# Kernel tuning notes

Hardware: AMD Instinct MI355X
Metric: run time of the kernel (lower is better)

Reference implementation:

```python
import jax, jax.numpy as jnp
import numpy as np
from jax import lax

B, CIN, H, W = 32, 256, 28, 28
COUT, KS, KEXP = 256, 3, 4
HIDDEN = int(CIN * 0.25)  # ratio hard-coded to 0.25 in the module


def setup_inputs() -> dict:
    key = jax.random.key(0)
    k1, k2, k3, k4 = jax.random.split(key, 4)
    x = jax.random.normal(k1, (B, CIN, H, W), dtype=jnp.float32)
    # SE (InvertedEx) params: fc1 (1x1 conv, no bias), fc2 (1x1 conv, bias)
    fc1_w = jax.random.normal(k2, (HIDDEN, CIN), dtype=jnp.float32) * np.float32(np.sqrt(2.0 / CIN))
    fc2_w = jax.random.normal(k3, (KEXP * COUT, HIDDEN), dtype=jnp.float32) * np.float32(np.sqrt(2.0 / HIDDEN))
    fc2_b = jnp.zeros((KEXP * COUT,), dtype=jnp.float32)
    # K expert conv kernels, he_std = sqrt(2) * (CIN*KS^2)^-0.5
    he_std = np.float32(np.sqrt(2.0) * (CIN * KS * KS) ** -0.5)
    weight = jax.random.normal(k4, (KEXP, COUT, CIN, KS, KS), dtype=jnp.float32) * he_std
    return {"x": x, "fc1_w": fc1_w, "fc2_w": fc2_w, "fc2_b": fc2_b, "weight": weight}


def reference(x, fc1_w, fc2_w, fc2_b, weight):
    # --- SE routing ---
    pooled = jnp.mean(x, axis=(2, 3))                        # [B, CIN]
    h = jax.nn.relu(pooled @ fc1_w.T)                        # [B, HIDDEN]
    y = (h @ fc2_w.T + fc2_b).reshape(B, KEXP, COUT)         # [B, K, COUT]
    prob = jax.nn.softmax(y / jnp.sqrt(jnp.float32(HIDDEN)), axis=1)  # softmax over K
    # --- aggregate per-sample kernels ---
    agg_w = jnp.einsum('bko,koihw->boihw', prob, weight)     # [B, COUT, CIN, KS, KS]
    # --- per-sample conv (batched implicit GEMM via vmap) ---
    def conv1(xi, wi):
        return lax.conv_general_dilated(
            xi[None], wi, window_strides=(1, 1), padding=((1, 1), (1, 1)),
            dimension_numbers=('NCHW', 'OIHW', 'NCHW'))[0]
    out = jax.vmap(conv1)(x, agg_w)                          # [B, COUT, H, W]
    return out
```

## Files before the change

kernel.cpp:

```cpp
#include <hip/hip_runtime.h>
#include <math.h>

#define B_    32
#define CIN_  256
#define HW_   784
#define H_    28
#define W_    28
#define COUT_ 256
#define KEXP_ 4
#define HID_  64

typedef short short8 __attribute__((ext_vector_type(8)));
typedef unsigned short ushort4v __attribute__((ext_vector_type(4)));
typedef unsigned short ushort8v __attribute__((ext_vector_type(8)));
typedef float floatx16 __attribute__((ext_vector_type(16)));

__device__ __forceinline__ unsigned short f2bf(float f) {
    union { float f; unsigned int u; } v; v.f = f;
    unsigned int r = (v.u + 0x7FFFu + ((v.u >> 16) & 1u)) >> 16;
    return (unsigned short)r;
}

__global__ __launch_bounds__(256) void xpose_pool_kernel(const float* __restrict__ x,
                                                         unsigned short* __restrict__ x_t,
                                                         float* __restrict__ partial) {
    __shared__ float tile[32][33];
    int bid = blockIdx.x;
    int b   = bid / 200;
    int rem = bid - b * 200;
    int icg = rem / 25;
    int pxt = rem % 25;
    int ic0 = icg * 32;
    int px0 = pxt * 32;
    int t = threadIdx.x;
    int c = t & 31, rr = t >> 5;
    #pragma unroll
    for (int r = 0; r < 4; ++r) {
        int icr = rr + r * 8;
        int px = px0 + c;
        float v = (px < HW_) ? x[((size_t)(b * CIN_ + ic0 + icr)) * HW_ + px] : 0.f;
        tile[icr][c] = v;
    }
    __syncthreads();
    #pragma unroll
    for (int r = 0; r < 4; ++r) {
        int pxr = rr + r * 8;
        int px = px0 + pxr;
        if (px < HW_)
            x_t[((size_t)b * HW_ + px) * CIN_ + ic0 + c] = f2bf(tile[c][pxr]);
    }
    if (t < 32) {
        float s = 0.f;
        #pragma unroll
        for (int cc = 0; cc < 32; ++cc) s += tile[t][cc];
        partial[((size_t)b * 25 + pxt) * CIN_ + ic0 + t] = s * (1.0f / HW_);
    }
}

__global__ __launch_bounds__(256) void pool_kernel(const float* __restrict__ x,
                                                   float* __restrict__ pooled) {
    int w = blockIdx.x * 4 + (threadIdx.x >> 6);
    int lane = threadIdx.x & 63;
    const float* p = x + (size_t)w * HW_;
    float s = 0.f;
    for (int i = lane; i < HW_; i += 64) s += p[i];
    for (int off = 32; off; off >>= 1) s += __shfl_down(s, off);
    if (lane == 0) pooled[w] = s * (1.0f / HW_);
}

__global__ __launch_bounds__(256) void se3_kernel(const float* __restrict__ partial,
                                                  const float* __restrict__ fc1_w,
                                                  const float* __restrict__ fc2_w,
                                                  const float* __restrict__ fc2_b,
                                                  float* __restrict__ prob) {
    __shared__ float pl[CIN_];
    __shared__ float h[HID_];
    __shared__ float wb[16640];
    int b = blockIdx.x, t = threadIdx.x;
    {
        float s = 0.f;
        for (int pt = 0; pt < 25; ++pt)
            s += partial[((size_t)b * 25 + pt) * CIN_ + t];
        pl[t] = s;
    }
    #pragma unroll
    for (int i = 0; i < 16; ++i) {
        int l = t + i * 256;
        float4 v = *(const float4*)(fc1_w + (size_t)l * 4);
        int r = l >> 6, cc = (l & 63) * 4;
        float* dst = &wb[r * 257 + cc];
        dst[0] = v.x; dst[1] = v.y; dst[2] = v.z; dst[3] = v.w;
    }
    __syncthreads();
    if (t < HID_) {
        float s = 0.f;
        const float* wr = &wb[t * 257];
        for (int c = 0; c < CIN_; ++c) s += pl[c] * wr[c];
        h[t] = fmaxf(s, 0.f);
    }
    float yk[KEXP_];
    for (int k = 0; k < KEXP_; ++k) {
        __syncthreads();
        #pragma unroll
        for (int i = 0; i < 16; ++i) {
            int l = t + i * 256;
            float4 v = *(const float4*)(fc2_w + (size_t)k * COUT_ * HID_ + (size_t)l * 4);
            int o = l >> 4, jj = (l & 15) * 4;
            float* dst = &wb[o * 65 + jj];
            dst[0] = v.x; dst[1] = v.y; dst[2] = v.z; dst[3] = v.w;
        }
        __syncthreads();
        float s = fc2_b[k * COUT_ + t];
        const float* wr = &wb[t * 65];
        #pragma unroll
        for (int j = 0; j < HID_; ++j) s += h[j] * wr[j];
        yk[k] = s * 0.125f;
    }
    float m = yk[0];
    for (int k = 1; k < KEXP_; ++k) m = fmaxf(m, yk[k]);
    float e[KEXP_], sum = 0.f;
    for (int k = 0; k < KEXP_; ++k) { e[k] = expf(yk[k] - m); sum += e[k]; }
    float inv = 1.0f / sum;
    for (int k = 0; k < KEXP_; ++k)
        prob[b * (KEXP_ * COUT_) + k * COUT_ + t] = e[k] * inv;
}

__global__ __launch_bounds__(256) void se2_kernel(const float* __restrict__ pooled,
                                                  const float* __restrict__ fc1_w,
                                                  const float* __restrict__ fc2_w,
                                                  const float* __restrict__ fc2_b,
                                                  float* __restrict__ prob) {
    __shared__ float pl[CIN_];
    __shared__ float h[HID_];
    __shared__ float wb[16640];
    int b = blockIdx.x, t = threadIdx.x;
    pl[t] = pooled[b * CIN_ + t];
    #pragma unroll
    for (int i = 0; i < 16; ++i) {
        int l = t + i * 256;
        float4 v = *(const float4*)(fc1_w + (size_t)l * 4);
        int r = l >> 6, cc = (l & 63) * 4;
        float* dst = &wb[r * 257 + cc];
        dst[0] = v.x; dst[1] = v.y; dst[2] = v.z; dst[3] = v.w;
    }
    __syncthreads();
    if (t < HID_) {
        float s = 0.f;
        const float* wr = &wb[t * 257];
        for (int c = 0; c < CIN_; ++c) s += pl[c] * wr[c];
        h[t] = fmaxf(s, 0.f);
    }
    float yk[KEXP_];
    for (int k = 0; k < KEXP_; ++k) {
        __syncthreads();
        #pragma unroll
        for (int i = 0; i < 16; ++i) {
            int l = t + i * 256;
            float4 v = *(const float4*)(fc2_w + (size_t)k * COUT_ * HID_ + (size_t)l * 4);
            int o = l >> 4, jj = (l & 15) * 4;
            float* dst = &wb[o * 65 + jj];
            dst[0] = v.x; dst[1] = v.y; dst[2] = v.z; dst[3] = v.w;
        }
        __syncthreads();
        float s = fc2_b[k * COUT_ + t];
        const float* wr = &wb[t * 65];
        #pragma unroll
        for (int j = 0; j < HID_; ++j) s += h[j] * wr[j];
        yk[k] = s * 0.125f;
    }
    float m = yk[0];
    for (int k = 1; k < KEXP_; ++k) m = fmaxf(m, yk[k]);
    float e[KEXP_], sum = 0.f;
    for (int k = 0; k < KEXP_; ++k) { e[k] = expf(yk[k] - m); sum += e[k]; }
    float inv = 1.0f / sum;
    for (int k = 0; k < KEXP_; ++k)
        prob[b * (KEXP_ * COUT_) + k * COUT_ + t] = e[k] * inv;
}

__global__ __launch_bounds__(256) void agg4_kernel(const float* __restrict__ weight,
                                                   const float* __restrict__ prob,
                                                   unsigned short* __restrict__ agg) {
    __shared__ float wlds[4][32][145];
    int gid = blockIdx.x;
    int og  = gid & 7;
    int icc = (gid >> 3) & 3;
    int kk  = (gid >> 5) & 3;
    int bh  = gid >> 7;
    int oc0 = og * 32;
    int ic0 = icc * 64 + kk * 16;
    int t = threadIdx.x;

    #pragma unroll
    for (int i = 0; i < 18; ++i) {
        int idx = t + i * 256;
        int k  = idx / 1152;
        int r  = idx - k * 1152;
        int oc = r / 36;
        int f4 = r - oc * 36;
        float4 v = *(const float4*)(weight + ((size_t)(k * COUT_ + oc0 + oc) * CIN_ + ic0) * 9 + f4 * 4);
        float* dst = &wlds[k][oc][f4 * 4];
        dst[0] = v.x; dst[1] = v.y; dst[2] = v.z; dst[3] = v.w;
    }

    int lane = t & 63, wv = t >> 6;
    int ml = lane & 31, kh = lane >> 5;

    float pbr[4][4];
    #pragma unroll
    for (int bi = 0; bi < 4; ++bi) {
        int b = bh * 16 + wv * 4 + bi;
        #pragma unroll
        for (int k = 0; k < 4; ++k)
            pbr[bi][k] = prob[(size_t)b * (KEXP_ * COUT_) + k * COUT_ + oc0 + ml];
    }
    __syncthreads();

    for (int rs = 0; rs < 9; ++rs) {
        float wreg[4][8];
        #pragma unroll
        for (int k = 0; k < 4; ++k)
            #pragma unroll
            for (int j = 0; j < 8; ++j)
                wreg[k][j] = wlds[k][ml][(kh * 8 + j) * 9 + rs];
        #pragma unroll
        for (int bi = 0; bi < 4; ++bi) {
            int b = bh * 16 + wv * 4 + bi;
            ushort8v pack;
            #pragma unroll
            for (int j = 0; j < 8; ++j) {
                float s = pbr[bi][0] * wreg[0][j] + pbr[bi][1] * wreg[1][j]
                        + pbr[bi][2] * wreg[2][j] + pbr[bi][3] * wreg[3][j];
                pack[j] = f2bf(s);
            }
            *(ushort8v*)(agg + (size_t)(b * 16 + icc * 4 + kk) * 36864
                             + (size_t)rs * 4096 + og * 512 + lane * 8) = pack;
        }
    }
}

__global__ __launch_bounds__(256, 1) void conv_mfma3_kernel(const unsigned short* __restrict__ x_t,
                                                            const unsigned short* __restrict__ agg,
                                                            float* __restrict__ out) {
    __shared__ __align__(16) short Xs[2][9 * 35 * 72];

    int gid = blockIdx.x;
    int b      = gid & 31;
    int half   = (gid >> 5) & 1;
    int oc0    = half * 128;
    int rowblk = gid >> 6;
    int py0 = rowblk * 7;

    int t = threadIdx.x;
    int lane = t & 63, w = t >> 6;
    int ml = lane & 31, kh = lane >> 5;
    int og = half * 4 + w;

    floatx16 acc[7];
    #pragma unroll
    for (int j = 0; j < 7; ++j)
        #pragma unroll
        for (int r = 0; r < 16; ++r) acc[j][r] = 0.f;

    const unsigned short* xtb = x_t + (size_t)b * HW_ * CIN_;
    const unsigned short* aln = agg + (size_t)b * 589824 + og * 512 + lane * 8;

    {
        #pragma unroll
        for (int i = 0; i < 10; ++i) {
            int l = t + i * 256;
            if (l < 2520) {
                int pos = l >> 3, g = l & 7;
                int row = pos / 35, col = pos - row * 35;
                int gy = py0 - 1 + row, gx = col - 1;
                short8 v = (short8)0;
                if ((unsigned)gy < 28u && (unsigned)gx < 28u)
                    v = *(const short8*)(xtb + ((size_t)(gy * W_ + gx)) * CIN_ + g * 8);
                *(short8*)&Xs[0][pos * 72 + g * 8] = v;
            }
        }
    }

    short8 Acur0, Acur1, Acur2, Anext0, Anext1, Anext2;
    Acur0 = *(const short8*)(aln);
    Acur1 = *(const short8*)(aln + 12288);
    Acur2 = *(const short8*)(aln + 24576);
    int dxn = 1, kkn = 0, icn = 0;

    __syncthreads();

    for (int c = 0; c < 4; ++c) {
        int ic0 = c * 64;
        const short* xb = &Xs[c & 1][0];

        short8 Xl[10];
        if (c < 3) {
            #pragma unroll
            for (int i = 0; i < 10; ++i) {
                int l = t + i * 256;
                short8 v = (short8)0;
                if (l < 2520) {
                    int pos = l >> 3, g = l & 7;
                    int row = pos / 35, col = pos - row * 35;
                    int gy = py0 - 1 + row, gx = col - 1;
                    if ((unsigned)gy < 28u && (unsigned)gx < 28u)
                        v = *(const short8*)(xtb + ((size_t)(gy * W_ + gx)) * CIN_ + ic0 + 64 + g * 8);
                }
                Xl[i] = v;
            }
        }

        for (int kk = 0; kk < 4; ++kk) {
            for (int dx = 0; dx < 3; ++dx) {
                if (icn < 256) {
                    const unsigned short* ap = aln + (size_t)(icn >> 6) * 147456
                                                   + (size_t)kkn * 36864 + (size_t)dxn * 4096;
                    Anext0 = *(const short8*)(ap);
                    Anext1 = *(const short8*)(ap + 12288);
                    Anext2 = *(const short8*)(ap + 24576);
                    ++dxn;
                    if (dxn == 3) { dxn = 0; ++kkn; if (kkn == 4) { kkn = 0; icn += 64; } }
                }
                int va = (ml + dx) * 72 + kk * 16 + kh * 8;
                #pragma unroll
                for (int r = 0; r < 9; ++r) {
                    short8 Bf = *(const short8*)&xb[r * 2520 + va];
                    if (r <= 6)
                        acc[r]     = __builtin_amdgcn_mfma_f32_32x32x16_bf16(Acur0, Bf, acc[r], 0, 0, 0);
                    if (r >= 1 && r - 1 <= 6)
                        acc[r - 1] = __builtin_amdgcn_mfma_f32_32x32x16_bf16(Acur1, Bf, acc[r - 1], 0, 0, 0);
                    if (r >= 2)
                        acc[r - 2] = __builtin_amdgcn_mfma_f32_32x32x16_bf16(Acur2, Bf, acc[r - 2], 0, 0, 0);
                }
                Acur0 = Anext0; Acur1 = Anext1; Acur2 = Anext2;
            }
        }

        if (c < 3) {
            short* dstb = &Xs[(c & 1) ^ 1][0];
            #pragma unroll
            for (int i = 0; i < 10; ++i) {
                int l = t + i * 256;
                if (l < 2520) {
                    int pos = l >> 3, g = l & 7;
                    *(short8*)&dstb[pos * 72 + g * 8] = Xl[i];
                }
            }
        }
        __syncthreads();
    }

    if (ml < W_) {
        #pragma unroll
        for (int j = 0; j < 7; ++j) {
            float* op = out + ((size_t)(b * COUT_ + oc0 + w * 32)) * HW_ + (py0 + j) * W_ + ml;
            #pragma unroll
            for (int r = 0; r < 16; ++r) {
                int ocd = (r & 3) + 8 * (r >> 2) + 4 * kh;
                op[(size_t)ocd * HW_] = acc[j][r];
            }
        }
    }
}

__global__ __launch_bounds__(256) void conv_kernel(const float* __restrict__ x,
                                                   const float* __restrict__ weight,
                                                   const float* __restrict__ prob,
                                                   float* __restrict__ out) {
    __shared__ float xs[30 * 30];
    __shared__ float wagg[8][32][12];
    __shared__ float pl[KEXP_][8];

    int b  = blockIdx.x >> 5;
    int o0 = (blockIdx.x & 31) * 8;
    int t  = threadIdx.x;

    if (t < 32) {
        int k = t >> 3, oc = t & 7;
        pl[k][oc] = prob[b * (KEXP_ * COUT_) + k * COUT_ + o0 + oc];
    }
    int p0 = t;
    int pr[4], pc[4];
    bool pv[4];
    #pragma unroll
    for (int j = 0; j < 4; ++j) {
        int p = p0 + j * 256;
        pv[j] = p < HW_;
        pr[j] = p / W_;
        pc[j] = p % W_;
    }
    float acc[8][4];
    #pragma unroll
    for (int oc = 0; oc < 8; ++oc)
        #pragma unroll
        for (int j = 0; j < 4; ++j) acc[oc][j] = 0.f;

    int aoc = t >> 5, aii = t & 31;

    for (int ic0 = 0; ic0 < CIN_; ic0 += 32) {
        __syncthreads();
        {
            float w9[9];
            #pragma unroll
            for (int j = 0; j < 9; ++j) w9[j] = 0.f;
            int i = ic0 + aii;
            #pragma unroll
            for (int k = 0; k < KEXP_; ++k) {
                float pk = pl[k][aoc];
                const float* wp = weight + ((size_t)(k * COUT_ + o0 + aoc) * CIN_ + i) * 9;
                #pragma unroll
                for (int j = 0; j < 9; ++j) w9[j] += pk * wp[j];
            }
            #pragma unroll
            for (int j = 0; j < 9; ++j) wagg[aoc][aii][j] = w9[j];
        }
        for (int ii = 0; ii < 32; ++ii) {
            int i = ic0 + ii;
            __syncthreads();
            const float* xp = x + (size_t)(b * CIN_ + i) * HW_;
            for (int e = t; e < 900; e += 256) {
                int ry = e / 30, cx = e - ry * 30;
                int gy = ry - 1, gx = cx - 1;
                float v = 0.f;
                if ((unsigned)gy < 28u && (unsigned)gx < 28u) v = xp[gy * W_ + gx];
                xs[e] = v;
            }
            __syncthreads();
            float xv[4][9];
            #pragma unroll
            for (int j = 0; j < 4; ++j) {
                if (pv[j]) {
                    const float* xr = &xs[pr[j] * 30 + pc[j]];
                    xv[j][0] = xr[0];  xv[j][1] = xr[1];  xv[j][2] = xr[2];
                    xv[j][3] = xr[30]; xv[j][4] = xr[31]; xv[j][5] = xr[32];
                    xv[j][6] = xr[60]; xv[j][7] = xr[61]; xv[j][8] = xr[62];
                } else {
                    #pragma unroll
                    for (int q = 0; q < 9; ++q) xv[j][q] = 0.f;
                }
            }
            #pragma unroll
            for (int oc = 0; oc < 8; ++oc) {
                float4 wa = *(const float4*)&wagg[oc][ii][0];
                float4 wb2 = *(const float4*)&wagg[oc][ii][4];
                float  wc = wagg[oc][ii][8];
                #pragma unroll
                for (int j = 0; j < 4; ++j) {
                    acc[oc][j] += xv[j][0] * wa.x + xv[j][1] * wa.y + xv[j][2] * wa.z
                                + xv[j][3] * wa.w + xv[j][4] * wb2.x + xv[j][5] * wb2.y
                                + xv[j][6] * wb2.z + xv[j][7] * wb2.w + xv[j][8] * wc;
                }
            }
        }
    }
    #pragma unroll
    for (int oc = 0; oc < 8; ++oc) {
        float* op = out + (size_t)(b * COUT_ + o0 + oc) * HW_ + p0;
        #pragma unroll
        for (int j = 0; j < 4; ++j)
            if (pv[j]) op[j * 256] = acc[oc][j];
    }
}

extern "C" void kernel_launch(void* const* d_in, const int* in_sizes, int n_in,
                              void* d_out, int out_size, void* d_ws, size_t ws_size,
                              hipStream_t stream) {
    const float* x     = (const float*)d_in[0];
    const float* fc1_w = (const float*)d_in[1];
    const float* fc2_w = (const float*)d_in[2];
    const float* fc2_b = (const float*)d_in[3];
    const float* weight= (const float*)d_in[4];
    float* out = (float*)d_out;

    char* ws = (char*)d_ws;
    float* prob = (float*)(ws);
    unsigned short* x_t = (unsigned short*)(ws + 131072);
    unsigned short* agg = (unsigned short*)(ws + 12976128);
    float* partial = (float*)(ws + 12976128);
    const size_t WS_NEED = 12976128 + (size_t)B_ * 9 * COUT_ * CIN_ * 2;

    if (ws_size >= WS_NEED) {
        xpose_pool_kernel<<<B_ * 8 * 25, 256, 0, stream>>>(x, x_t, partial);
        se3_kernel<<<B_, 256, 0, stream>>>(partial, fc1_w, fc2_w, fc2_b, prob);
        agg4_kernel<<<256, 256, 0, stream>>>(weight, prob, agg);
        conv_mfma3_kernel<<<256, 256, 0, stream>>>(x_t, agg, out);
    } else {
        float* pooled = (float*)(ws + 131072);
        pool_kernel<<<(B_ * CIN_) / 4, 256, 0, stream>>>(x, pooled);
        se2_kernel<<<B_, 256, 0, stream>>>(pooled, fc1_w, fc2_w, fc2_b, prob);
        conv_kernel<<<B_ * (COUT_ / 8), 256, 0, stream>>>(x, weight, prob, out);
    }
}
```

Before: 149.2 us.

## Fuse expert-weight aggregation into conv kernel, dropping per-sample bf16 weight buffer

```diff
diff --git a/kernel.cpp b/kernel.cpp
--- a/kernel.cpp
+++ b/kernel.cpp
@@ -14,6 +14,7 @@
 typedef unsigned short ushort4v __attribute__((ext_vector_type(4)));
 typedef unsigned short ushort8v __attribute__((ext_vector_type(8)));
 typedef float floatx16 __attribute__((ext_vector_type(16)));
+typedef float float8v __attribute__((ext_vector_type(8)));
 
 __device__ __forceinline__ unsigned short f2bf(float f) {
     union { float f; unsigned int u; } v; v.f = f;
@@ -177,15 +178,13 @@
         prob[b * (KEXP_ * COUT_) + k * COUT_ + t] = e[k] * inv;
 }
 
-__global__ __launch_bounds__(256) void agg4_kernel(const float* __restrict__ weight,
-                                                   const float* __restrict__ prob,
-                                                   unsigned short* __restrict__ agg) {
+__global__ __launch_bounds__(256) void wfrag_kernel(const float* __restrict__ weight,
+                                                    float* __restrict__ wf) {
     __shared__ float wlds[4][32][145];
     int gid = blockIdx.x;
     int og  = gid & 7;
     int icc = (gid >> 3) & 3;
-    int kk  = (gid >> 5) & 3;
-    int bh  = gid >> 7;
+    int kk  = gid >> 5;
     int oc0 = og * 32;
     int ic0 = icc * 64 + kk * 16;
     int t = threadIdx.x;
@@ -201,45 +200,24 @@
         float* dst = &wlds[k][oc][f4 * 4];
         dst[0] = v.x; dst[1] = v.y; dst[2] = v.z; dst[3] = v.w;
     }
+    __syncthreads();
 
     int lane = t & 63, wv = t >> 6;
     int ml = lane & 31, kh = lane >> 5;
 
-    float pbr[4][4];
-    #pragma unroll
-    for (int bi = 0; bi < 4; ++bi) {
-        int b = bh * 16 + wv * 4 + bi;
-        #pragma unroll
-        for (int k = 0; k < 4; ++k)
-            pbr[bi][k] = prob[(size_t)b * (KEXP_ * COUT_) + k * COUT_ + oc0 + ml];
-    }
-    __syncthreads();
-
     for (int rs = 0; rs < 9; ++rs) {
-        float wreg[4][8];
-        #pragma unroll
-        for (int k = 0; k < 4; ++k)
-            #pragma unroll
-            for (int j = 0; j < 8; ++j)
-                wreg[k][j] = wlds[k][ml][(kh * 8 + j) * 9 + rs];
-        #pragma unroll
-        for (int bi = 0; bi < 4; ++bi) {
-            int b = bh * 16 + wv * 4 + bi;
-            ushort8v pack;
-            #pragma unroll
-            for (int j = 0; j < 8; ++j) {
-                float s = pbr[bi][0] * wreg[0][j] + pbr[bi][1] * wreg[1][j]
-                        + pbr[bi][2] * wreg[2][j] + pbr[bi][3] * wreg[3][j];
-                pack[j] = f2bf(s);
-            }
-            *(ushort8v*)(agg + (size_t)(b * 16 + icc * 4 + kk) * 36864
-                             + (size_t)rs * 4096 + og * 512 + lane * 8) = pack;
-        }
-    }
-}
-
-__global__ __launch_bounds__(256, 1) void conv_mfma3_kernel(const unsigned short* __restrict__ x_t,
-                                                            const unsigned short* __restrict__ agg,
+        float8v v;
+        #pragma unroll
+        for (int j = 0; j < 8; ++j)
+            v[j] = wlds[wv][ml][(kh * 8 + j) * 9 + rs];
+        *(float8v*)(wf + ((size_t)(((wv * 4 + icc) * 4 + kk) * 9 + rs)) * 4096
+                       + og * 512 + lane * 8) = v;
+    }
+}
+
+__global__ __launch_bounds__(256, 1) void conv_mfma4_kernel(const unsigned short* __restrict__ x_t,
+                                                            const float* __restrict__ wf,
+                                                            const float* __restrict__ prob,
                                                             float* __restrict__ out) {
     __shared__ __align__(16) short Xs[2][9 * 35 * 72];
 
@@ -262,7 +240,12 @@
         for (int r = 0; r < 16; ++r) acc[j][r] = 0.f;
 
     const unsigned short* xtb = x_t + (size_t)b * HW_ * CIN_;
-    const unsigned short* aln = agg + (size_t)b * 589824 + og * 512 + lane * 8;
+    const float* wfl = wf + og * 512 + lane * 8;
+
+    float p0 = prob[(size_t)b * (KEXP_ * COUT_) + 0 * COUT_ + oc0 + w * 32 + ml];
+    float p1 = prob[(size_t)b * (KEXP_ * COUT_) + 1 * COUT_ + oc0 + w * 32 + ml];
+    float p2 = prob[(size_t)b * (KEXP_ * COUT_) + 2 * COUT_ + oc0 + w * 32 + ml];
+    float p3 = prob[(size_t)b * (KEXP_ * COUT_) + 3 * COUT_ + oc0 + w * 32 + ml];
 
     {
         #pragma unroll
@@ -280,10 +263,12 @@
         }
     }
 
-    short8 Acur0, Acur1, Acur2, Anext0, Anext1, Anext2;
-    Acur0 = *(const short8*)(aln);
-    Acur1 = *(const short8*)(aln + 12288);
-    Acur2 = *(const short8*)(aln + 24576);
+    float8v Rw[3][4];
+    #pragma unroll
+    for (int tap = 0; tap < 3; ++tap)
+        #pragma unroll
+        for (int k = 0; k < 4; ++k)
+            Rw[tap][k] = *(const float8v*)(wfl + (size_t)k * 589824 + (size_t)tap * 12288);
     int dxn = 1, kkn = 0, icn = 0;
 
     __syncthreads();
@@ -311,12 +296,29 @@
 
         for (int kk = 0; kk < 4; ++kk) {
             for (int dx = 0; dx < 3; ++dx) {
+                short8 A0, A1, A2;
+                {
+                    #pragma unroll
+                    for (int tap = 0; tap < 3; ++tap) {
+                        short8 Ax;
+                        #pragma unroll
+                        for (int j = 0; j < 8; ++j) {
+                            float s = p0 * Rw[tap][0][j] + p1 * Rw[tap][1][j]
+                                    + p2 * Rw[tap][2][j] + p3 * Rw[tap][3][j];
+                            Ax[j] = (short)f2bf(s);
+                        }
+                        if (tap == 0) A0 = Ax; else if (tap == 1) A1 = Ax; else A2 = Ax;
+                    }
+                }
                 if (icn < 256) {
-                    const unsigned short* ap = aln + (size_t)(icn >> 6) * 147456
-                                                   + (size_t)kkn * 36864 + (size_t)dxn * 4096;
-                    Anext0 = *(const short8*)(ap);
-                    Anext1 = *(const short8*)(ap + 12288);
-                    Anext2 = *(const short8*)(ap + 24576);
+                    const float* ap = wfl + (size_t)(icn >> 6) * 147456
+                                          + (size_t)kkn * 36864 + (size_t)dxn * 4096;
+                    #pragma unroll
+                    for (int tap = 0; tap < 3; ++tap)
+                        #pragma unroll
+                        for (int k = 0; k < 4; ++k)
+                            Rw[tap][k] = *(const float8v*)(ap + (size_t)k * 589824
+                                                              + (size_t)tap * 12288);
                     ++dxn;
                     if (dxn == 3) { dxn = 0; ++kkn; if (kkn == 4) { kkn = 0; icn += 64; } }
                 }
@@ -325,13 +327,12 @@
                 for (int r = 0; r < 9; ++r) {
                     short8 Bf = *(const short8*)&xb[r * 2520 + va];
                     if (r <= 6)
-                        acc[r]     = __builtin_amdgcn_mfma_f32_32x32x16_bf16(Acur0, Bf, acc[r], 0, 0, 0);
+                        acc[r]     = __builtin_amdgcn_mfma_f32_32x32x16_bf16(A0, Bf, acc[r], 0, 0, 0);
                     if (r >= 1 && r - 1 <= 6)
-                        acc[r - 1] = __builtin_amdgcn_mfma_f32_32x32x16_bf16(Acur1, Bf, acc[r - 1], 0, 0, 0);
+                        acc[r - 1] = __builtin_amdgcn_mfma_f32_32x32x16_bf16(A1, Bf, acc[r - 1], 0, 0, 0);
                     if (r >= 2)
-                        acc[r - 2] = __builtin_amdgcn_mfma_f32_32x32x16_bf16(Acur2, Bf, acc[r - 2], 0, 0, 0);
-                }
-                Acur0 = Anext0; Acur1 = Anext1; Acur2 = Anext2;
+                        acc[r - 2] = __builtin_amdgcn_mfma_f32_32x32x16_bf16(A2, Bf, acc[r - 2], 0, 0, 0);
+                }
             }
         }
 
@@ -474,15 +475,15 @@
     char* ws = (char*)d_ws;
     float* prob = (float*)(ws);
     unsigned short* x_t = (unsigned short*)(ws + 131072);
-    unsigned short* agg = (unsigned short*)(ws + 12976128);
     float* partial = (float*)(ws + 12976128);
-    const size_t WS_NEED = 12976128 + (size_t)B_ * 9 * COUT_ * CIN_ * 2;
+    float* wf = (float*)(ws + 13795328);
+    const size_t WS_NEED = 13795328 + (size_t)KEXP_ * COUT_ * CIN_ * 9 * 4;
 
     if (ws_size >= WS_NEED) {
         xpose_pool_kernel<<<B_ * 8 * 25, 256, 0, stream>>>(x, x_t, partial);
         se3_kernel<<<B_, 256, 0, stream>>>(partial, fc1_w, fc2_w, fc2_b, prob);
-        agg4_kernel<<<256, 256, 0, stream>>>(weight, prob, agg);
-        conv_mfma3_kernel<<<256, 256, 0, stream>>>(x_t, agg, out);
+        wfrag_kernel<<<128, 256, 0, stream>>>(weight, wf);
+        conv_mfma4_kernel<<<256, 256, 0, stream>>>(x_t, wf, prob, out);
     } else {
         float* pooled = (float*)(ws + 131072);
         pool_kernel<<<(B_ * CIN_) / 4, 256, 0, stream>>>(x, pooled);
```

Result: slower. 168.1 us (+12.7%).
